# Kernel tuning notes

Hardware: AMD Instinct MI355X
Metric: run time of the kernel (lower is better)

The kernel has to match this reference:

```python
import jax, jax.numpy as jnp
import numpy as np

NUM_BLOCKS = 8
BLOCK_SIZE = 96  # 768 // 8
LAMBDA = 0.01


def softshrink(x, lam=LAMBDA):
    return jnp.sign(x) * jnp.maximum(jnp.abs(x) - lam, 0.0)


def setup_inputs() -> dict:
    key = jax.random.key(0)
    k1, k2, k3 = jax.random.split(key, 3)
    B, H, W, C = 4, 128, 128, 768
    # xavier_uniform bound for [block_size, block_size] fan_in=fan_out=96
    bound = float(np.sqrt(6.0 / (BLOCK_SIZE + BLOCK_SIZE)))
    x = jax.random.normal(k1, (B, H, W, C), dtype=jnp.float32)
    w1 = jax.random.uniform(k2, (2, NUM_BLOCKS, BLOCK_SIZE, BLOCK_SIZE), minval=-bound, maxval=bound, dtype=jnp.float32)
    w2 = jax.random.uniform(k3, (2, NUM_BLOCKS, BLOCK_SIZE, BLOCK_SIZE), minval=-bound, maxval=bound, dtype=jnp.float32)
    b1 = jnp.zeros((2, NUM_BLOCKS, BLOCK_SIZE), dtype=jnp.float32)
    b2 = jnp.zeros((2, NUM_BLOCKS, BLOCK_SIZE), dtype=jnp.float32)
    return {"x": x, "w1": w1, "w2": w2, "b1": b1, "b2": b2}


def reference(x, w1, w2, b1, b2):
    bias = x
    B, H, W, C = x.shape
    xf = jnp.fft.rfft2(x.astype(jnp.float32), axes=(1, 2), norm='ortho')  # [B,H,W//2+1,C] complex
    Wf = xf.shape[2]
    xf = xf.reshape(B, H, Wf, NUM_BLOCKS, BLOCK_SIZE)
    xr, xi = jnp.real(xf), jnp.imag(xf)
    # first complex block-diagonal MLP layer
    o1r = jnp.einsum('bhwki,kio->bhwko', xr, w1[0]) - jnp.einsum('bhwki,kio->bhwko', xi, w1[1]) + b1[0]
    o1i = jnp.einsum('bhwki,kio->bhwko', xi, w1[0]) + jnp.einsum('bhwki,kio->bhwko', xr, w1[1]) + b1[1]
    o1r = softshrink(o1r)
    o1i = softshrink(o1i)
    # second layer
    o2r = jnp.einsum('bhwki,kio->bhwko', o1r, w2[0]) - jnp.einsum('bhwki,kio->bhwko', o1i, w2[1]) + b2[0]
    o2i = jnp.einsum('bhwki,kio->bhwko', o1i, w2[0]) + jnp.einsum('bhwki,kio->bhwko', o1r, w2[1]) + b2[1]
    o2r = softshrink(o2r)
    o2i = softshrink(o2i)
    yf = (o2r + 1j * o2i).reshape(B, H, Wf, C)
    y = jnp.fft.irfft2(yf, s=(H, W), axes=(1, 2), norm='ortho')
    return y.astype(x.dtype) + bias
```

## Files before the change

kernel.cpp:

```cpp
#include <hip/hip_runtime.h>
#include <cmath>

#define PI_D 3.14159265358979323846

static constexpr int B_ = 4, H_ = 128, W_ = 128, C_ = 768, WF = 65;
static constexpr size_t PLANE = (size_t)B_ * H_ * WF * C_;
static constexpr float LAMBDA_ = 0.01f;

using short8   = __attribute__((ext_vector_type(8))) short;
using floatx16 = __attribute__((ext_vector_type(16))) float;

__device__ __forceinline__ float2 cmul(float2 a, float2 b) {
  return make_float2(a.x * b.x - a.y * b.y, a.x * b.y + a.y * b.x);
}
__device__ __forceinline__ unsigned short f2bfu(float f) {
  union { float f; unsigned u; } v; v.f = f;
  unsigned r = v.u + 0x7FFFu + ((v.u >> 16) & 1u);
  return (unsigned short)(r >> 16);
}
__device__ __forceinline__ float bf2f(unsigned short u) {
  union { unsigned u; float f; } v; v.u = (unsigned)u << 16;
  return v.f;
}
__device__ __forceinline__ float softshrink(float v) {
  return v > LAMBDA_ ? v - LAMBDA_ : (v < -LAMBDA_ ? v + LAMBDA_ : 0.0f);
}

template<int SIGN, int S>
__device__ __forceinline__ void fft64_stage(float2* z, const float2* tw) {
  constexpr int half = 1 << S;
  #pragma unroll
  for (int g = 0; g < 32; ++g) {
    const int j  = g & (half - 1);
    const int i0 = ((g >> S) << (S + 1)) + j;
    const int i1 = i0 + half;
    float2 w = tw[j << (5 - S)];
    if (SIGN > 0) w.y = -w.y;
    float2 t = cmul(w, z[i1]);
    float2 a = z[i0];
    z[i0] = make_float2(a.x + t.x, a.y + t.y);
    z[i1] = make_float2(a.x - t.x, a.y - t.y);
  }
}
template<int SIGN>
__device__ __forceinline__ void fft64(float2* z, const float2* tw) {
  #pragma unroll
  for (int i = 0; i < 64; ++i) {
    const int j = ((i >> 5) & 1) | (((i >> 4) & 1) << 1) | (((i >> 3) & 1) << 2)
                | (((i >> 2) & 1) << 3) | (((i >> 1) & 1) << 4) | ((i & 1) << 5);
    if (i < j) { float2 t = z[i]; z[i] = z[j]; z[j] = t; }
  }
  fft64_stage<SIGN, 0>(z, tw);
  fft64_stage<SIGN, 1>(z, tw);
  fft64_stage<SIGN, 2>(z, tw);
  fft64_stage<SIGN, 3>(z, tw);
  fft64_stage<SIGN, 4>(z, tw);
  fft64_stage<SIGN, 5>(z, tw);
}

__global__ void k_init_tw(float2* tw64, float2* tw128) {
  int t = threadIdx.x;
  if (t < 32) {
    double th = -2.0 * PI_D * (double)t / 64.0;
    tw64[t] = make_float2((float)cos(th), (float)sin(th));
  }
  if (t < 65) {
    double th = -PI_D * (double)t / 64.0;
    tw128[t] = make_float2((float)cos(th), (float)sin(th));
  }
}

__global__ __launch_bounds__(256) void k_wconv(
    const float* __restrict__ w1, const float* __restrict__ w2,
    unsigned short* __restrict__ wbf) {
  const int flat = blockIdx.x * 256 + threadIdx.x;
  const int i  = flat % 104;
  const int t2 = flat / 104;
  const int o  = t2 % 96;
  const int t3 = t2 / 96;
  const int ri = t3 & 1;
  const int t4 = t3 >> 1;
  const int kb = t4 & 7;
  const int layer = t4 >> 3;
  const float* w = layer ? w2 : w1;
  unsigned short v = 0;
  if (i < 96) v = f2bfu(w[((size_t)(ri * 8 + kb) * 96 + i) * 96 + o]);
  wbf[flat] = v;
}

__global__ __launch_bounds__(256) void k_rfft_w(
    const float* __restrict__ x,
    unsigned short* __restrict__ Sr, unsigned short* __restrict__ Si,
    const float2* __restrict__ tw64g, const float2* __restrict__ tw128g) {
  __shared__ float2 stw64[32];
  __shared__ float2 stw128[65];
  const int tid = threadIdx.x;
  if (tid < 32) stw64[tid]  = tw64g[tid];
  if (tid < 65) stw128[tid] = tw128g[tid];
  __syncthreads();
  const int blk = blockIdx.x;
  const int cc = blk % 3, bh = blk / 3;
  const int c = cc * 256 + tid;
  const float* xp = x + (size_t)bh * (W_ * C_) + c;
  float2 z[64];
  #pragma unroll
  for (int n = 0; n < 64; ++n) {
    z[n].x = xp[(size_t)(2 * n) * C_];
    z[n].y = xp[(size_t)(2 * n + 1) * C_];
  }
  fft64<-1>(z, stw64);
  const size_t obase = (size_t)bh * (WF * C_) + c;
  #pragma unroll
  for (int k = 0; k <= 64; ++k) {
    float2 a  = z[k & 63];
    float2 bq = z[(64 - k) & 63];
    float2 ze = make_float2(0.5f * (a.x + bq.x), 0.5f * (a.y - bq.y));
    float2 d  = make_float2(0.5f * (a.x - bq.x), 0.5f * (a.y + bq.y));
    float2 zo = make_float2(d.y, -d.x);
    float2 w  = stw128[k];
    float2 X  = make_float2(ze.x + w.x * zo.x - w.y * zo.y,
                            ze.y + w.x * zo.y + w.y * zo.x);
    Sr[obase + (size_t)k * C_] = f2bfu(X.x);
    Si[obase + (size_t)k * C_] = f2bfu(X.y);
  }
}

static constexpr int L_W = 512, L_P = 20480, L_S = 47104;
static constexpr int L_BYTES = 73728 * 2;

__global__ __launch_bounds__(256) void k_mid(
    unsigned short* __restrict__ Sr, unsigned short* __restrict__ Si,
    const unsigned short* __restrict__ wbf,
    const float* __restrict__ b1, const float* __restrict__ b2,
    const float2* __restrict__ tw64g, const float2* __restrict__ tw128g) {
  extern __shared__ unsigned short lds[];
  float2* stw64  = (float2*)lds;
  float2* stw128 = (float2*)(lds + 128);
  const int tid = threadIdx.x;
  if (tid < 32) stw64[tid]  = tw64g[tid];
  if (tid < 65) stw128[tid] = tw128g[tid];

  const int kb = blockIdx.x & 7;
  const int t2 = blockIdx.x >> 3;
  const int wf = t2 % 65, b = t2 / 65;
  const size_t hstr = (size_t)WF * C_;
  const size_t gb0  = ((size_t)b * H_ * WF + wf) * (size_t)C_ + (size_t)kb * 96;

  {
    const unsigned short* g = wbf + (size_t)kb * 19968;
    #pragma unroll
    for (int it = 0; it < 10; ++it) {
      int idx = tid + it * 256;
      if (idx < 2496) *(short8*)&lds[L_W + idx * 8] = *(const short8*)&g[idx * 8];
    }
  }
  #pragma unroll
  for (int it = 0; it < 48; ++it) {
    const int u = it * 256 + tid;
    const int p = (it >= 24);
    const int v = u - p * 6144;
    const int row = v / 48, cp = v - row * 48;
    const unsigned short* src = (p ? Si : Sr) + gb0 + (size_t)row * hstr + cp * 2;
    *(unsigned int*)&lds[L_P + p * 13312 + row * 104 + cp * 2] =
        *(const unsigned int*)src;
  }
  __syncthreads();

  const int wv = tid >> 6, lane = tid & 63;
  const int half = wv >> 1;
  const int ch = tid & 127;
  const bool act = ch < 96;
  float2* Efd = (float2*)&lds[L_S];

  float2 z[64];
  if (act) {
    #pragma unroll
    for (int n = 0; n < 64; ++n) {
      const int row = 2 * n + half;
      z[n].x = bf2f(lds[L_P + row * 104 + ch]);
      z[n].y = bf2f(lds[L_P + 13312 + row * 104 + ch]);
    }
    fft64<-1>(z, stw64);
    if (half == 0) {
      #pragma unroll
      for (int k = 0; k < 64; ++k) Efd[k * 96 + ch] = z[k];
    } else {
      #pragma unroll
      for (int k = 0; k < 64; ++k) z[k] = cmul(stw128[k], z[k]);
    }
  }
  __syncthreads();
  if (act && half == 1) {
    const float sc = 1.0f / 128.0f;
    #pragma unroll
    for (int k = 0; k < 64; ++k) {
      const float2 E = Efd[k * 96 + ch];
      const float2 t = z[k];
      lds[L_P + k * 104 + ch]                 = f2bfu((E.x + t.x) * sc);
      lds[L_P + 13312 + k * 104 + ch]         = f2bfu((E.y + t.y) * sc);
      lds[L_P + (k + 64) * 104 + ch]          = f2bfu((E.x - t.x) * sc);
      lds[L_P + 13312 + (k + 64) * 104 + ch]  = f2bfu((E.y - t.y) * sc);
    }
  }
  __syncthreads();

  const int mh = wv & 1, nh = wv >> 1;
  const int n32 = lane & 31, khalf = lane >> 5;
  const unsigned short* wr = lds + L_W;
  const unsigned short* wi = lds + L_W + 9984;

  #pragma unroll
  for (int mt = 0; mt < 2; ++mt) {
    const int p0 = mt * 64;
    floatx16 acc[3];
    #pragma unroll
    for (int t = 0; t < 3; ++t)
      #pragma unroll
      for (int e = 0; e < 16; ++e) acc[t][e] = 0.0f;
    const int arow = p0 + mh * 32 + n32;
    #pragma unroll
    for (int kk = 0; kk < 12; ++kk) {
      const int kr = kk >= 6;
      const int kloc = (kk - kr * 6) * 16 + khalf * 8;
      short8 afr = *(const short8*)&lds[L_P + kr * 13312 + arow * 104 + kloc];
      const unsigned short* bb = (kr != nh) ? wi : wr;
      #pragma unroll
      for (int nt = 0; nt < 3; ++nt) {
        short8 bfr = *(const short8*)&bb[(nt * 32 + n32) * 104 + kloc];
        if (kr && !nh) {
          union { short8 s; int v[4]; } u; u.s = bfr;
          u.v[0] ^= 0x80008000; u.v[1] ^= 0x80008000;
          u.v[2] ^= 0x80008000; u.v[3] ^= 0x80008000;
          bfr = u.s;
        }
        acc[nt] = __builtin_amdgcn_mfma_f32_32x32x16_bf16(afr, bfr, acc[nt], 0, 0, 0);
      }
    }
    #pragma unroll
    for (int nt = 0; nt < 3; ++nt) {
      const int o = nt * 32 + n32;
      const float bs = b1[(nh * 8 + kb) * 96 + o];
      #pragma unroll
      for (int reg = 0; reg < 16; ++reg) {
        const int m = p0 + mh * 32 + (reg & 3) + 8 * (reg >> 2) + 4 * khalf;
        lds[L_S + nh * 13312 + m * 104 + o] = f2bfu(softshrink(acc[nt][reg] + bs));
      }
    }
  }
  __syncthreads();

  {
    const unsigned short* g = wbf + (size_t)(8 + kb) * 19968;
    #pragma unroll
    for (int it = 0; it < 10; ++it) {
      int idx = tid + it * 256;
      if (idx < 2496) *(short8*)&lds[L_W + idx * 8] = *(const short8*)&g[idx * 8];
    }
  }
  __syncthreads();

  #pragma unroll
  for (int mt = 0; mt < 2; ++mt) {
    const int p0 = mt * 64;
    floatx16 acc[3];
    #pragma unroll
    for (int t = 0; t < 3; ++t)
      #pragma unroll
      for (int e = 0; e < 16; ++e) acc[t][e] = 0.0f;
    const int arow = p0 + mh * 32 + n32;
    #pragma unroll
    for (int kk = 0; kk < 12; ++kk) {
      const int kr = kk >= 6;
      const int kloc = (kk - kr * 6) * 16 + khalf * 8;
      short8 afr = *(const short8*)&lds[L_S + kr * 13312 + arow * 104 + kloc];
      const unsigned short* bb = (kr != nh) ? wi : wr;
      #pragma unroll
      for (int nt = 0; nt < 3; ++nt) {
        short8 bfr = *(const short8*)&bb[(nt * 32 + n32) * 104 + kloc];
        if (kr && !nh) {
          union { short8 s; int v[4]; } u; u.s = bfr;
          u.v[0] ^= 0x80008000; u.v[1] ^= 0x80008000;
          u.v[2] ^= 0x80008000; u.v[3] ^= 0x80008000;
          bfr = u.s;
        }
        acc[nt] = __builtin_amdgcn_mfma_f32_32x32x16_bf16(afr, bfr, acc[nt], 0, 0, 0);
      }
    }
    #pragma unroll
    for (int nt = 0; nt < 3; ++nt) {
      const int o = nt * 32 + n32;
      const float bs = b2[(nh * 8 + kb) * 96 + o];
      #pragma unroll
      for (int reg = 0; reg < 16; ++reg) {
        const int m = p0 + mh * 32 + (reg & 3) + 8 * (reg >> 2) + 4 * khalf;
        lds[L_P + nh * 13312 + m * 104 + o] = f2bfu(softshrink(acc[nt][reg] + bs));
      }
    }
  }
  __syncthreads();

  if (act) {
    #pragma unroll
    for (int n = 0; n < 64; ++n) {
      const int row = 2 * n + half;
      z[n].x = bf2f(lds[L_P + row * 104 + ch]);
      z[n].y = bf2f(lds[L_P + 13312 + row * 104 + ch]);
    }
    fft64<1>(z, stw64);
    if (half == 0) {
      #pragma unroll
      for (int k = 0; k < 64; ++k) Efd[k * 96 + ch] = z[k];
    } else {
      #pragma unroll
      for (int k = 0; k < 64; ++k) {
        float2 w = stw128[k]; w.y = -w.y;
        z[k] = cmul(w, z[k]);
      }
    }
  }
  __syncthreads();
  if (act && half == 1) {
    #pragma unroll
    for (int k = 0; k < 64; ++k) {
      const float2 E = Efd[k * 96 + ch];
      const float2 t = z[k];
      const size_t g0 = gb0 + (size_t)k * hstr + ch;
      const size_t g1 = gb0 + (size_t)(k + 64) * hstr + ch;
      Sr[g0] = f2bfu(E.x + t.x); Si[g0] = f2bfu(E.y + t.y);
      Sr[g1] = f2bfu(E.x - t.x); Si[g1] = f2bfu(E.y - t.y);
    }
  }
}

__global__ __launch_bounds__(256) void k_irfft_w(
    const unsigned short* __restrict__ Sr, const unsigned short* __restrict__ Si,
    const float* __restrict__ xin, float* __restrict__ y,
    const float2* __restrict__ tw64g, const float2* __restrict__ tw128g) {
  __shared__ float2 stw64[32];
  __shared__ float2 stw128[65];
  const int tid = threadIdx.x;
  if (tid < 32) stw64[tid]  = tw64g[tid];
  if (tid < 65) stw128[tid] = tw128g[tid];
  __syncthreads();
  const int blk = blockIdx.x;
  const int cc = blk % 3, bh = blk / 3;
  const int c = cc * 256 + tid;
  const size_t ibase = (size_t)bh * (WF * C_) + c;
  float2 z[64];
  {
    float x0r  = bf2f(Sr[ibase]);
    float x64r = bf2f(Sr[ibase + (size_t)64 * C_]);
    z[0] = make_float2(0.5f * (x0r + x64r), 0.5f * (x0r - x64r));
  }
  #pragma unroll
  for (int k = 1; k <= 32; ++k) {
    float2 a, b;
    a.x = bf2f(Sr[ibase + (size_t)k * C_]);        a.y = bf2f(Si[ibase + (size_t)k * C_]);
    b.x = bf2f(Sr[ibase + (size_t)(64 - k) * C_]); b.y = bf2f(Si[ibase + (size_t)(64 - k) * C_]);
    float2 s = make_float2(0.5f * (a.x + b.x), 0.5f * (a.y - b.y));
    float2 d = make_float2(0.5f * (a.x - b.x), 0.5f * (a.y + b.y));
    float2 w = stw128[k]; w.y = -w.y;
    float2 zo = cmul(w, d);
    z[k] = make_float2(s.x - zo.y, s.y + zo.x);
    if (k < 32) z[64 - k] = make_float2(s.x + zo.y, zo.x - s.y);
  }
  fft64<1>(z, stw64);
  const float* xb = xin + (size_t)bh * (W_ * C_) + c;
  float*       yb = y   + (size_t)bh * (W_ * C_) + c;
  #pragma unroll
  for (int n = 0; n < 64; ++n) {
    yb[(size_t)(2 * n) * C_]     = z[n].x * (1.0f / 64.0f) + xb[(size_t)(2 * n) * C_];
    yb[(size_t)(2 * n + 1) * C_] = z[n].y * (1.0f / 64.0f) + xb[(size_t)(2 * n + 1) * C_];
  }
}

extern "C" void kernel_launch(void* const* d_in, const int* in_sizes, int n_in,
                              void* d_out, int out_size, void* d_ws, size_t ws_size,
                              hipStream_t stream) {
  const float* x  = (const float*)d_in[0];
  const float* w1 = (const float*)d_in[1];
  const float* w2 = (const float*)d_in[2];
  const float* b1 = (const float*)d_in[3];
  const float* b2 = (const float*)d_in[4];
  float* y = (float*)d_out;

  float2* tw64  = (float2*)d_ws;
  float2* tw128 = tw64 + 32;
  unsigned short* wbf = (unsigned short*)((char*)d_ws + 1024);
  unsigned short* Sr  = (unsigned short*)((char*)d_ws + (1 << 20));
  unsigned short* Si  = Sr + PLANE;

  static bool attr_done = false;
  if (!attr_done) {
    hipFuncSetAttribute((const void*)k_mid,
                        hipFuncAttributeMaxDynamicSharedMemorySize, L_BYTES);
    attr_done = true;
  }

  k_init_tw<<<1, 128, 0, stream>>>(tw64, tw128);
  k_wconv<<<dim3(1248), dim3(256), 0, stream>>>(w1, w2, wbf);
  k_rfft_w<<<dim3(B_ * H_ * 3), dim3(256), 0, stream>>>(x, Sr, Si, tw64, tw128);
  k_mid<<<dim3(260 * 8), dim3(256), L_BYTES, stream>>>(Sr, Si, wbf, b1, b2, tw64, tw128);
  k_irfft_w<<<dim3(B_ * H_ * 3), dim3(256), 0, stream>>>(Sr, Si, x, y, tw64, tw128);
}
```

Measured before the change: 776.0 us.

## Shrink k_mid LDS footprint for two blocks per CU using shuffles and global weights

Weights are no longer staged in LDS; MFMA B-fragments are read straight from global (L2-cached) memory, and the weight buffer drops its padding to 96 columns. The FFT butterfly combine between the two half-sequences now uses cross-lane shuffles instead of an LDS scratch buffer plus a barrier, with channel-to-lane mapping changed to 24 active channels per wave. Layer-1 output is staged per 64-row M-tile, so LDS falls from about 147KB to about 78KB and launch bounds request 2 blocks per CU. The aim is higher occupancy and fewer barriers, at the cost of global-memory latency on B-fragment loads, a 100-element row stride that may cause more LDS bank conflicts, and only 24 of 32 lanes per half-wave doing FFT work.

```diff
diff --git a/kernel.cpp b/kernel.cpp
--- a/kernel.cpp
+++ b/kernel.cpp
@@ -74,8 +74,8 @@
     const float* __restrict__ w1, const float* __restrict__ w2,
     unsigned short* __restrict__ wbf) {
   const int flat = blockIdx.x * 256 + threadIdx.x;
-  const int i  = flat % 104;
-  const int t2 = flat / 104;
+  const int i  = flat % 96;
+  const int t2 = flat / 96;
   const int o  = t2 % 96;
   const int t3 = t2 / 96;
   const int ri = t3 & 1;
@@ -83,9 +83,7 @@
   const int kb = t4 & 7;
   const int layer = t4 >> 3;
   const float* w = layer ? w2 : w1;
-  unsigned short v = 0;
-  if (i < 96) v = f2bfu(w[((size_t)(ri * 8 + kb) * 96 + i) * 96 + o]);
-  wbf[flat] = v;
+  wbf[flat] = f2bfu(w[((size_t)(ri * 8 + kb) * 96 + i) * 96 + o]);
 }
 
 __global__ __launch_bounds__(256) void k_rfft_w(
@@ -125,10 +123,10 @@
   }
 }
 
-static constexpr int L_W = 512, L_P = 20480, L_S = 47104;
-static constexpr int L_BYTES = 73728 * 2;
-
-__global__ __launch_bounds__(256) void k_mid(
+static constexpr int LP_ = 512, LO_ = 26112;
+static constexpr int L_BYTES = 38912 * 2;
+
+__global__ __launch_bounds__(256, 2) void k_mid(
     unsigned short* __restrict__ Sr, unsigned short* __restrict__ Si,
     const unsigned short* __restrict__ wbf,
     const float* __restrict__ b1, const float* __restrict__ b2,
@@ -146,70 +144,54 @@
   const size_t hstr = (size_t)WF * C_;
   const size_t gb0  = ((size_t)b * H_ * WF + wf) * (size_t)C_ + (size_t)kb * 96;
 
-  {
-    const unsigned short* g = wbf + (size_t)kb * 19968;
-    #pragma unroll
-    for (int it = 0; it < 10; ++it) {
-      int idx = tid + it * 256;
-      if (idx < 2496) *(short8*)&lds[L_W + idx * 8] = *(const short8*)&g[idx * 8];
-    }
-  }
-  #pragma unroll
-  for (int it = 0; it < 48; ++it) {
+  #pragma unroll
+  for (int it = 0; it < 24; ++it) {
     const int u = it * 256 + tid;
-    const int p = (it >= 24);
-    const int v = u - p * 6144;
-    const int row = v / 48, cp = v - row * 48;
-    const unsigned short* src = (p ? Si : Sr) + gb0 + (size_t)row * hstr + cp * 2;
-    *(unsigned int*)&lds[L_P + p * 13312 + row * 104 + cp * 2] =
-        *(const unsigned int*)src;
+    const int p = (it >= 12);
+    const int v = u - p * 3072;
+    const int row = v / 24, cp = v - row * 24;
+    const unsigned short* src = (p ? Si : Sr) + gb0 + (size_t)row * hstr + cp * 4;
+    *(uint2*)&lds[LP_ + p * 12800 + row * 100 + cp * 4] = *(const uint2*)src;
   }
   __syncthreads();
 
   const int wv = tid >> 6, lane = tid & 63;
-  const int half = wv >> 1;
-  const int ch = tid & 127;
-  const bool act = ch < 96;
-  float2* Efd = (float2*)&lds[L_S];
+  const int c32 = lane & 31, half = lane >> 5;
+  const int ch = wv * 24 + c32;
+  const bool act = c32 < 24;
 
   float2 z[64];
   if (act) {
     #pragma unroll
     for (int n = 0; n < 64; ++n) {
       const int row = 2 * n + half;
-      z[n].x = bf2f(lds[L_P + row * 104 + ch]);
-      z[n].y = bf2f(lds[L_P + 13312 + row * 104 + ch]);
+      z[n].x = bf2f(lds[LP_ + row * 100 + ch]);
+      z[n].y = bf2f(lds[LP_ + 12800 + row * 100 + ch]);
     }
     fft64<-1>(z, stw64);
-    if (half == 0) {
-      #pragma unroll
-      for (int k = 0; k < 64; ++k) Efd[k * 96 + ch] = z[k];
-    } else {
-      #pragma unroll
-      for (int k = 0; k < 64; ++k) z[k] = cmul(stw128[k], z[k]);
-    }
-  }
-  __syncthreads();
-  if (act && half == 1) {
     const float sc = 1.0f / 128.0f;
     #pragma unroll
     for (int k = 0; k < 64; ++k) {
-      const float2 E = Efd[k * 96 + ch];
-      const float2 t = z[k];
-      lds[L_P + k * 104 + ch]                 = f2bfu((E.x + t.x) * sc);
-      lds[L_P + 13312 + k * 104 + ch]         = f2bfu((E.y + t.y) * sc);
-      lds[L_P + (k + 64) * 104 + ch]          = f2bfu((E.x - t.x) * sc);
-      lds[L_P + 13312 + (k + 64) * 104 + ch]  = f2bfu((E.y - t.y) * sc);
+      float2 mine = z[k];
+      if (half) mine = cmul(stw128[k], mine);
+      float2 oth;
+      oth.x = __shfl_xor(mine.x, 32, 64);
+      oth.y = __shfl_xor(mine.y, 32, 64);
+      float2 X = half ? make_float2(oth.x - mine.x, oth.y - mine.y)
+                      : make_float2(mine.x + oth.x, mine.y + oth.y);
+      const int row = k + half * 64;
+      lds[LP_ + row * 100 + ch]         = f2bfu(X.x * sc);
+      lds[LP_ + 12800 + row * 100 + ch] = f2bfu(X.y * sc);
     }
   }
   __syncthreads();
 
   const int mh = wv & 1, nh = wv >> 1;
   const int n32 = lane & 31, khalf = lane >> 5;
-  const unsigned short* wr = lds + L_W;
-  const unsigned short* wi = lds + L_W + 9984;
-
-  #pragma unroll
+  const unsigned short* wL1 = wbf + (size_t)kb * 18432;
+  const unsigned short* wL2 = wbf + (size_t)(8 + kb) * 18432;
+
+  #pragma unroll 1
   for (int mt = 0; mt < 2; ++mt) {
     const int p0 = mt * 64;
     floatx16 acc[3];
@@ -222,11 +204,11 @@
     for (int kk = 0; kk < 12; ++kk) {
       const int kr = kk >= 6;
       const int kloc = (kk - kr * 6) * 16 + khalf * 8;
-      short8 afr = *(const short8*)&lds[L_P + kr * 13312 + arow * 104 + kloc];
-      const unsigned short* bb = (kr != nh) ? wi : wr;
+      short8 afr = *(const short8*)&lds[LP_ + kr * 12800 + arow * 100 + kloc];
+      const unsigned short* bb = wL1 + (kr != nh) * 9216;
       #pragma unroll
       for (int nt = 0; nt < 3; ++nt) {
-        short8 bfr = *(const short8*)&bb[(nt * 32 + n32) * 104 + kloc];
+        short8 bfr = *(const short8*)&bb[(nt * 32 + n32) * 96 + kloc];
         if (kr && !nh) {
           union { short8 s; int v[4]; } u; u.s = bfr;
           u.v[0] ^= 0x80008000; u.v[1] ^= 0x80008000;
@@ -242,41 +224,26 @@
       const float bs = b1[(nh * 8 + kb) * 96 + o];
       #pragma unroll
       for (int reg = 0; reg < 16; ++reg) {
-        const int m = p0 + mh * 32 + (reg & 3) + 8 * (reg >> 2) + 4 * khalf;
-        lds[L_S + nh * 13312 + m * 104 + o] = f2bfu(softshrink(acc[nt][reg] + bs));
+        const int m0 = mh * 32 + (reg & 3) + 8 * (reg >> 2) + 4 * khalf;
+        lds[LO_ + nh * 6400 + m0 * 100 + o] = f2bfu(softshrink(acc[nt][reg] + bs));
       }
     }
-  }
-  __syncthreads();
-
-  {
-    const unsigned short* g = wbf + (size_t)(8 + kb) * 19968;
-    #pragma unroll
-    for (int it = 0; it < 10; ++it) {
-      int idx = tid + it * 256;
-      if (idx < 2496) *(short8*)&lds[L_W + idx * 8] = *(const short8*)&g[idx * 8];
-    }
-  }
-  __syncthreads();
-
-  #pragma unroll
-  for (int mt = 0; mt < 2; ++mt) {
-    const int p0 = mt * 64;
-    floatx16 acc[3];
+    __syncthreads();
+
     #pragma unroll
     for (int t = 0; t < 3; ++t)
       #pragma unroll
       for (int e = 0; e < 16; ++e) acc[t][e] = 0.0f;
-    const int arow = p0 + mh * 32 + n32;
+    const int arow2 = mh * 32 + n32;
     #pragma unroll
     for (int kk = 0; kk < 12; ++kk) {
       const int kr = kk >= 6;
       const int kloc = (kk - kr * 6) * 16 + khalf * 8;
-      short8 afr = *(const short8*)&lds[L_S + kr * 13312 + arow * 104 + kloc];
-      const unsigned short* bb = (kr != nh) ? wi : wr;
+      short8 afr = *(const short8*)&lds[LO_ + kr * 6400 + arow2 * 100 + kloc];
+      const unsigned short* bb = wL2 + (kr != nh) * 9216;
       #pragma unroll
       for (int nt = 0; nt < 3; ++nt) {
-        short8 bfr = *(const short8*)&bb[(nt * 32 + n32) * 104 + kloc];
+        short8 bfr = *(const short8*)&bb[(nt * 32 + n32) * 96 + kloc];
         if (kr && !nh) {
           union { short8 s; int v[4]; } u; u.s = bfr;
           u.v[0] ^= 0x80008000; u.v[1] ^= 0x80008000;
@@ -292,42 +259,32 @@
       const float bs = b2[(nh * 8 + kb) * 96 + o];
       #pragma unroll
       for (int reg = 0; reg < 16; ++reg) {
-        const int m = p0 + mh * 32 + (reg & 3) + 8 * (reg >> 2) + 4 * khalf;
-        lds[L_P + nh * 13312 + m * 104 + o] = f2bfu(softshrink(acc[nt][reg] + bs));
+        const int m0 = mh * 32 + (reg & 3) + 8 * (reg >> 2) + 4 * khalf;
+        lds[LP_ + nh * 12800 + (p0 + m0) * 100 + o] = f2bfu(softshrink(acc[nt][reg] + bs));
       }
     }
-  }
-  __syncthreads();
+    __syncthreads();
+  }
 
   if (act) {
     #pragma unroll
     for (int n = 0; n < 64; ++n) {
       const int row = 2 * n + half;
-      z[n].x = bf2f(lds[L_P + row * 104 + ch]);
-      z[n].y = bf2f(lds[L_P + 13312 + row * 104 + ch]);
+      z[n].x = bf2f(lds[LP_ + row * 100 + ch]);
+      z[n].y = bf2f(lds[LP_ + 12800 + row * 100 + ch]);
     }
     fft64<1>(z, stw64);
-    if (half == 0) {
-      #pragma unroll
-      for (int k = 0; k < 64; ++k) Efd[k * 96 + ch] = z[k];
-    } else {
-      #pragma unroll
-      for (int k = 0; k < 64; ++k) {
-        float2 w = stw128[k]; w.y = -w.y;
-        z[k] = cmul(w, z[k]);
-      }
-    }
-  }
-  __syncthreads();
-  if (act && half == 1) {
     #pragma unroll
     for (int k = 0; k < 64; ++k) {
-      const float2 E = Efd[k * 96 + ch];
-      const float2 t = z[k];
-      const size_t g0 = gb0 + (size_t)k * hstr + ch;
-      const size_t g1 = gb0 + (size_t)(k + 64) * hstr + ch;
-      Sr[g0] = f2bfu(E.x + t.x); Si[g0] = f2bfu(E.y + t.y);
-      Sr[g1] = f2bfu(E.x - t.x); Si[g1] = f2bfu(E.y - t.y);
+      float2 mine = z[k];
+      if (half) { float2 w = stw128[k]; w.y = -w.y; mine = cmul(w, mine); }
+      float2 oth;
+      oth.x = __shfl_xor(mine.x, 32, 64);
+      oth.y = __shfl_xor(mine.y, 32, 64);
+      float2 X = half ? make_float2(oth.x - mine.x, oth.y - mine.y)
+                      : make_float2(mine.x + oth.x, mine.y + oth.y);
+      const size_t g = gb0 + (size_t)(k + half * 64) * hstr + ch;
+      Sr[g] = f2bfu(X.x); Si[g] = f2bfu(X.y);
     }
   }
 }
@@ -398,7 +355,7 @@
   }
 
   k_init_tw<<<1, 128, 0, stream>>>(tw64, tw128);
-  k_wconv<<<dim3(1248), dim3(256), 0, stream>>>(w1, w2, wbf);
+  k_wconv<<<dim3(1152), dim3(256), 0, stream>>>(w1, w2, wbf);
   k_rfft_w<<<dim3(B_ * H_ * 3), dim3(256), 0, stream>>>(x, Sr, Si, tw64, tw128);
   k_mid<<<dim3(260 * 8), dim3(256), L_BYTES, stream>>>(Sr, Si, wbf, b1, b2, tw64, tw128);
   k_irfft_w<<<dim3(B_ * H_ * 3), dim3(256), 0, stream>>>(Sr, Si, x, y, tw64, tw128);
```

New measurement: 1.221 ms. 57.4% more time.
